# Kernel tuning notes

Measured on AMD Instinct MI355X. Metric: run time of the kernel, lower is better.

The kernel has to match this reference:

```python
import jax, jax.numpy as jnp
import numpy as np
import math

NUM_HEADS = 4
HIDDEN = 256
HEAD_DIM = HIDDEN // NUM_HEADS
NEG = jnp.finfo(jnp.float32).min


def setup_inputs() -> dict:
    key = jax.random.key(0)
    ks = jax.random.split(key, 8)
    B, Q, K = 4, 2048, 2048
    q_hidden_states = jax.random.normal(ks[0], (B, Q, HIDDEN), dtype=jnp.float32)
    k_hidden_states = jax.random.normal(ks[1], (B, K, HIDDEN), dtype=jnp.float32)
    attention_mask = jnp.zeros((B, 1, Q, K), dtype=jnp.float32)
    align_mask = jax.random.randint(ks[2], (B, K, Q), 0, 2, dtype=jnp.int32)
    s = 1.0 / math.sqrt(HIDDEN)
    Wq = jax.random.normal(ks[3], (HIDDEN, HIDDEN), dtype=jnp.float32) * s
    Wk = jax.random.normal(ks[4], (HIDDEN, HIDDEN), dtype=jnp.float32) * s
    Wv = jax.random.normal(ks[5], (HIDDEN, HIDDEN), dtype=jnp.float32) * s
    Wo = jax.random.normal(ks[6], (HIDDEN, HIDDEN), dtype=jnp.float32) * s
    return {"q_hidden_states": q_hidden_states, "k_hidden_states": k_hidden_states,
            "attention_mask": attention_mask, "align_mask": align_mask,
            "Wq": Wq, "Wk": Wk, "Wv": Wv, "Wo": Wo}


def reference(q_hidden_states, k_hidden_states, attention_mask, align_mask, Wq, Wk, Wv, Wo):
    B, Q, _ = q_hidden_states.shape
    K = k_hidden_states.shape[1]
    # torch Linear: y = x @ W.T  -> [B, S, H, D]
    q = (q_hidden_states @ Wq.T).reshape(B, Q, NUM_HEADS, HEAD_DIM)
    k = (k_hidden_states @ Wk.T).reshape(B, K, NUM_HEADS, HEAD_DIM)
    v = (k_hidden_states @ Wv.T).reshape(B, K, NUM_HEADS, HEAD_DIM)
    # scores: [B, H, Q, K]
    scores = jnp.einsum('bqhd,bkhd->bhqk', q, k) / math.sqrt(HEAD_DIM)
    # additive mask + clamp to finfo min
    scores = jnp.maximum(scores + attention_mask, NEG)
    # align_mask: (B, K, Q) -> (B, 1, Q, K); masked_fill where == 0
    am = jnp.transpose(align_mask, (0, 2, 1))[:, None, :, :]
    scores = jnp.where(am == 0, NEG, scores)
    scores = jnp.maximum(scores, NEG)
    probs = jax.nn.softmax(scores.astype(jnp.float32), axis=-1).astype(q.dtype)
    attn = jnp.einsum('bhqk,bkhd->bqhd', probs, v).reshape(B, Q, HIDDEN)
    return attn @ Wo.T
```

## Files before the change

kernel.cpp:

```cpp
#include <hip/hip_runtime.h>

#define NEGF -3.402823466e38f
#define MASKED_F -3.38953139e38f
#define LOG2E 1.44269504088896f
#define DEFER_THR 8.0f

typedef __attribute__((ext_vector_type(8))) short bf16x8;
typedef __attribute__((ext_vector_type(4))) float f32x4;
typedef __attribute__((ext_vector_type(4))) unsigned short u16x4;
typedef __attribute__((ext_vector_type(2))) unsigned int u32x2;

__device__ __forceinline__ unsigned short f2bf(float f) {
  unsigned u = __builtin_bit_cast(unsigned, f);
  u += 0x7fffu + ((u >> 16) & 1u);
  return (unsigned short)(u >> 16);
}

#define GLOAD_LDS16(gsrc, ldst)                                                     \
  __builtin_amdgcn_global_load_lds(                                                 \
      (const __attribute__((address_space(1))) void*)(gsrc),                        \
      (__attribute__((address_space(3))) void*)(ldst), 16, 0, 0)

#define OFF_QH  0u
#define OFF_KH  2097152u
#define OFF_W   4194304u
#define OFF_QP  4456448u
#define OFF_KP  6553600u
#define OFF_VT  8650752u
#define OFF_ATT 10747904u
#define OFF_BM  12845056u
#define OFF_FLAG 13893632u
#define USHORT_USED 13893664u

__global__ __launch_bounds__(256) void k_convert(
    const float* __restrict__ qh, const float* __restrict__ kh,
    const float* __restrict__ w0, const float* __restrict__ w1,
    const float* __restrict__ w2, const float* __restrict__ w3,
    unsigned short* __restrict__ dst) {
  int v = blockIdx.x * 256 + threadIdx.x;
  const float* src;
  if (v < 524288)       src = qh + (size_t)v * 4;
  else if (v < 1048576) src = kh + ((size_t)v - 524288) * 4;
  else {
    int t = v - 1048576;
    int which = t >> 14;
    const float* w = (which == 0) ? w0 : (which == 1) ? w1 : (which == 2) ? w2 : w3;
    src = w + (size_t)(t & 16383) * 4;
  }
  f32x4 x = *(const f32x4*)src;
  u16x4 o;
  o[0] = f2bf(x[0]); o[1] = f2bf(x[1]); o[2] = f2bf(x[2]); o[3] = f2bf(x[3]);
  *(u16x4*)(dst + (size_t)v * 4) = o;
}

__global__ __launch_bounds__(256) void k_bitpack(const int* __restrict__ al,
                                                 unsigned long long* __restrict__ bm,
                                                 int* __restrict__ flag) {
  int wi = blockIdx.x * 256 + threadIdx.x;
  if (wi == 0) *flag = 0;
  int q = wi & 2047;
  int k64 = (wi >> 11) & 31;
  int b = wi >> 16;
  const int* base = al + ((size_t)(b * 2048 + k64 * 64)) * 2048 + q;
  unsigned long long word = 0;
#pragma unroll
  for (int k = 0; k < 64; ++k)
    if (base[(size_t)k * 2048] != 0) word |= 1ull << k;
  bm[wi] = word;
}

__global__ __launch_bounds__(256) void k_amcheck(const float* __restrict__ am,
                                                 int* __restrict__ flag) {
  const f32x4* p = (const f32x4*)am;
  size_t tid = (size_t)blockIdx.x * 256 + threadIdx.x;
  unsigned nz = 0;
#pragma unroll
  for (int j = 0; j < 8; ++j) {
    f32x4 v = p[tid + (size_t)j * 524288];
    nz |= (v[0] != 0.f) | (v[1] != 0.f) | (v[2] != 0.f) | (v[3] != 0.f);
  }
  if (__any(nz)) {
    if ((threadIdx.x & 63) == 0) atomicOr(flag, 1);
  }
}

__global__ __launch_bounds__(256) void k_proj(unsigned short* __restrict__ ws) {
  int bid = blockIdx.x;
  int mat = bid / 512;
  int rem = bid - mat * 512;
  int mt = rem >> 2, nt = rem & 3;
  int tid = threadIdx.x, w = tid >> 6, lane = tid & 63;
  int l15 = lane & 15, l4 = lane >> 4;

  const unsigned short* X = ws + (mat == 0 ? OFF_QH : OFF_KH);
  const unsigned short* W = ws + OFF_W + (size_t)mat * 65536;

  int i0 = mt * 64 + w * 16;
  int arow = i0 + l15;
  int koff = l4 * 8;

  f32x4 acc[4] = {};
  for (int ks = 0; ks < 8; ++ks) {
    bf16x8 a = *(const bf16x8*)(X + (size_t)arow * 256 + ks * 32 + koff);
#pragma unroll
    for (int ct = 0; ct < 4; ++ct) {
      bf16x8 bb = *(const bf16x8*)(W + (size_t)(nt * 64 + ct * 16 + l15) * 256 + ks * 32 + koff);
      acc[ct] = __builtin_amdgcn_mfma_f32_16x16x32_bf16(a, bb, acc[ct], 0, 0, 0);
    }
  }

  unsigned short* Qp = ws + OFF_QP;
  unsigned short* Kp = ws + OFF_KP;
  unsigned short* Vt = ws + OFF_VT;
  int rbase = i0 + l4 * 4;
#pragma unroll
  for (int ct = 0; ct < 4; ++ct) {
#pragma unroll
    for (int r = 0; r < 4; ++r) {
      int row = rbase + r;
      int b = row >> 11, s = row & 2047;
      int d = ct * 16 + l15;
      float v = acc[ct][r];
      if (mat == 0)      Qp[((size_t)(b * 4 + nt) * 2048 + s) * 64 + d] = f2bf(v * (0.125f * LOG2E));
      else if (mat == 1) Kp[((size_t)(b * 4 + nt) * 2048 + s) * 64 + d] = f2bf(v);
      else               Vt[((size_t)(b * 4 + nt) * 64 + d) * 2048 + s] = f2bf(v);
    }
  }
}

template <int NS>
__global__ __launch_bounds__(256) void k_attn(unsigned short* __restrict__ ws,
    const float* __restrict__ am, const unsigned long long* __restrict__ bm,
    const int* __restrict__ amflag,
    float* __restrict__ po, float* __restrict__ pm, float* __restrict__ pl) {
  constexpr int LOG = (NS == 4) ? 2 : (NS == 2) ? 1 : 0;
  constexpr int SPAN = 2048 / NS;

  __shared__ __align__(16) unsigned short Kb[2][4096];
  __shared__ __align__(16) unsigned short Vb[2][4096];
  __shared__ __align__(16) unsigned short plds[4][1024];

  int bid = blockIdx.x;
  int sp = bid & (NS - 1);
  int qt = (bid >> LOG) & 31;
  int bh = bid >> (LOG + 5);
  int b = bh >> 2, h = bh & 3;
  int tid = threadIdx.x, w = tid >> 6, lane = tid & 63;
  int l15 = lane & 15, l4 = lane >> 4;
  int q0 = qt * 64 + w * 16;

  const bool hasam = (*amflag != 0);

  const unsigned short* Qp = ws + OFF_QP;
  const unsigned short* Kp = ws + OFF_KP + (size_t)bh * 2048 * 64;
  const unsigned short* Vt = ws + OFF_VT + (size_t)bh * 64 * 2048;
  const float* amq = am + ((size_t)(b * 2048 + q0 + l15)) * 2048;
  const unsigned long long* bmq = bm + (size_t)b * 65536 + q0 + l15;

  int srow = lane >> 3;
  int scol = ((lane & 7) ^ srow) * 8;
  int c0 = w * 2;

  bf16x8 qf0 = *(const bf16x8*)(Qp + ((size_t)bh * 2048 + q0 + l15) * 64 + l4 * 8);
  bf16x8 qf1 = *(const bf16x8*)(Qp + ((size_t)bh * 2048 + q0 + l15) * 64 + 32 + l4 * 8);

  f32x4 o[4] = {};
  float mrun = -__builtin_inff();
  float lpart = 0.f;
  int s0 = l4 * 4;

  int kk0 = sp * SPAN;
#pragma unroll
  for (int c2 = 0; c2 < 2; ++c2) {
    int c = c0 + c2;
    GLOAD_LDS16(Kp + (size_t)(kk0 + c * 8 + srow) * 64 + scol, &Kb[0][c * 512]);
    GLOAD_LDS16(Vt + (size_t)(c * 8 + srow) * 2048 + kk0 + scol, &Vb[0][c * 512]);
  }
  __syncthreads();

  int cur = 0;
  for (int kk = kk0; kk < kk0 + SPAN; kk += 64) {
    if (kk + 64 < kk0 + SPAN) {
#pragma unroll
      for (int c2 = 0; c2 < 2; ++c2) {
        int c = c0 + c2;
        GLOAD_LDS16(Kp + (size_t)(kk + 64 + c * 8 + srow) * 64 + scol, &Kb[cur ^ 1][c * 512]);
        GLOAD_LDS16(Vt + (size_t)(c * 8 + srow) * 2048 + (kk + 64) + scol, &Vb[cur ^ 1][c * 512]);
      }
    }
    unsigned long long wbits = bmq[(size_t)(kk >> 6) * 2048];
    unsigned blo = (unsigned)wbits, bhi = (unsigned)(wbits >> 32);
    f32x4 a0{}, a1{}, a2{}, a3{};
    if (hasam) {
      a0 = *(const f32x4*)(amq + kk + 0 * 16 + s0);
      a1 = *(const f32x4*)(amq + kk + 1 * 16 + s0);
      a2 = *(const f32x4*)(amq + kk + 2 * 16 + s0);
      a3 = *(const f32x4*)(amq + kk + 3 * 16 + s0);
    }

    f32x4 sfr[4];
    __builtin_amdgcn_s_setprio(1);
#pragma unroll
    for (int kt = 0; kt < 4; ++kt) {
      int row = kt * 16 + l15;
      int sw = l15 & 7;
      bf16x8 k0 = *(const bf16x8*)&Kb[cur][row * 64 + ((l4 ^ sw) * 8)];
      bf16x8 k1 = *(const bf16x8*)&Kb[cur][row * 64 + (((4 + l4) ^ sw) * 8)];
      f32x4 acc = {};
      acc = __builtin_amdgcn_mfma_f32_16x16x32_bf16(k0, qf0, acc, 0, 0, 0);
      acc = __builtin_amdgcn_mfma_f32_16x16x32_bf16(k1, qf1, acc, 0, 0, 0);
      sfr[kt] = acc;
    }
    __builtin_amdgcn_s_setprio(0);

#pragma unroll
    for (int kt = 0; kt < 4; ++kt) {
      unsigned half = (kt & 2) ? bhi : blo;
      int base = (kt & 1) ? 16 + s0 : s0;
      f32x4 a = (kt == 0) ? a0 : (kt == 1) ? a1 : (kt == 2) ? a2 : a3;
#pragma unroll
      for (int r = 0; r < 4; ++r) {
        float sc = sfr[kt][r];
        if (hasam) sc = fmaf(a[r], LOG2E, sc);
        sfr[kt][r] = ((half >> (base + r)) & 1u) ? sc : MASKED_F;
      }
    }

    float pmax = sfr[0][0];
#pragma unroll
    for (int kt = 0; kt < 4; ++kt)
#pragma unroll
      for (int r = 0; r < 4; ++r) pmax = fmaxf(pmax, sfr[kt][r]);
    pmax = fmaxf(pmax, __shfl_xor(pmax, 16));
    pmax = fmaxf(pmax, __shfl_xor(pmax, 32));

    if (__any(pmax > mrun + DEFER_THR)) {
      float mnew = fmaxf(mrun, pmax);
      float sfac = exp2f(mrun - mnew);
      mrun = mnew;
      lpart *= sfac;
#pragma unroll
      for (int r = 0; r < 4; ++r) {
        float sf = __shfl(sfac, l4 * 4 + r);
        o[0][r] *= sf; o[1][r] *= sf; o[2][r] *= sf; o[3][r] *= sf;
      }
    }

    float ls = 0.f;
#pragma unroll
    for (int kt = 0; kt < 4; ++kt)
#pragma unroll
      for (int r = 0; r < 4; ++r) {
        float e = exp2f(sfr[kt][r] - mrun);
        sfr[kt][r] = e;
        ls += e;
      }
    lpart += ls;

#pragma unroll
    for (int kt = 0; kt < 4; ++kt) {
      unsigned lo, hi;
      asm("v_cvt_pk_bf16_f32 %0, %1, %2" : "=v"(lo) : "v"(sfr[kt][0]), "v"(sfr[kt][1]));
      asm("v_cvt_pk_bf16_f32 %0, %1, %2" : "=v"(hi) : "v"(sfr[kt][2]), "v"(sfr[kt][3]));
      int chunk = kt * 2 + (l4 >> 1);
      int addr = l15 * 64 + (((chunk) ^ (l15 & 7)) << 3) + ((l4 & 1) << 2);
      u32x2 pk; pk[0] = lo; pk[1] = hi;
      *(u32x2*)&plds[w][addr] = pk;
    }

    __builtin_amdgcn_s_setprio(1);
#pragma unroll
    for (int ks = 0; ks < 2; ++ks) {
      int chnk = ks * 4 + l4;
      bf16x8 pa = *(const bf16x8*)&plds[w][l15 * 64 + ((chnk ^ (l15 & 7)) << 3)];
#pragma unroll
      for (int dt = 0; dt < 4; ++dt) {
        int row = dt * 16 + l15;
        bf16x8 vf = *(const bf16x8*)&Vb[cur][row * 64 + (((ks * 4 + l4) ^ (l15 & 7)) * 8)];
        o[dt] = __builtin_amdgcn_mfma_f32_16x16x32_bf16(pa, vf, o[dt], 0, 0, 0);
      }
    }
    __builtin_amdgcn_s_setprio(0);

    __syncthreads();
    cur ^= 1;
  }

  float lsum = lpart;
  lsum += __shfl_xor(lsum, 16);
  lsum += __shfl_xor(lsum, 32);

  if constexpr (NS == 1) {
    unsigned short* attnb = ws + OFF_ATT;
#pragma unroll
    for (int r = 0; r < 4; ++r) {
      float inv = 1.0f / __shfl(lsum, l4 * 4 + r);
      int qrow = q0 + l4 * 4 + r;
#pragma unroll
      for (int dt = 0; dt < 4; ++dt)
        attnb[(size_t)(b * 2048 + qrow) * 256 + h * 64 + dt * 16 + l15] = f2bf(o[dt][r] * inv);
    }
  } else {
    float* pob = po + (((size_t)sp * 16 + bh) * 2048) * 64;
#pragma unroll
    for (int r = 0; r < 4; ++r) {
      int qrow = q0 + l4 * 4 + r;
#pragma unroll
      for (int dt = 0; dt < 4; ++dt)
        pob[(size_t)qrow * 64 + dt * 16 + l15] = o[dt][r];
    }
    if (l4 == 0) {
      pm[(size_t)sp * 32768 + bh * 2048 + q0 + l15] = mrun;
      pl[(size_t)sp * 32768 + bh * 2048 + q0 + l15] = lsum;
    }
  }
}

template <int NS>
__global__ __launch_bounds__(256) void k_combine(const float* __restrict__ po,
    const float* __restrict__ pm, const float* __restrict__ pl,
    unsigned short* __restrict__ attnb) {
  int t = blockIdx.x * 256 + threadIdx.x;
  int d = t & 63;
  int row = t >> 6;

  float m[NS], l[NS];
  float M = -__builtin_inff();
#pragma unroll
  for (int sp = 0; sp < NS; ++sp) {
    m[sp] = pm[(size_t)sp * 32768 + row];
    l[sp] = pl[(size_t)sp * 32768 + row];
    M = fmaxf(M, m[sp]);
  }
  float denom = 0.f, acc = 0.f;
#pragma unroll
  for (int sp = 0; sp < NS; ++sp) {
    float wgt = exp2f(m[sp] - M);
    denom += l[sp] * wgt;
    acc += po[((size_t)sp * 32768 + row) * 64 + d] * wgt;
  }
  float val = acc / denom;
  int bh = row >> 11, qrow = row & 2047;
  int b = bh >> 2, h = bh & 3;
  attnb[((size_t)(b * 2048 + qrow)) * 256 + h * 64 + d] = f2bf(val);
}

__global__ __launch_bounds__(256) void k_oproj(const unsigned short* __restrict__ ws,
                                               float* __restrict__ out) {
  int bid = blockIdx.x;
  int mt = bid >> 2, nt = bid & 3;
  int tid = threadIdx.x, w = tid >> 6, lane = tid & 63;
  int l15 = lane & 15, l4 = lane >> 4;

  const unsigned short* A = ws + OFF_ATT;
  const unsigned short* W = ws + OFF_W + 3u * 65536u;
  int i0 = mt * 64 + w * 16;

  f32x4 acc[4] = {};
  for (int ks = 0; ks < 8; ++ks) {
    bf16x8 a = *(const bf16x8*)(A + (size_t)(i0 + l15) * 256 + ks * 32 + l4 * 8);
#pragma unroll
    for (int ct = 0; ct < 4; ++ct) {
      bf16x8 bb = *(const bf16x8*)(W + (size_t)(nt * 64 + ct * 16 + l15) * 256 + ks * 32 + l4 * 8);
      acc[ct] = __builtin_amdgcn_mfma_f32_16x16x32_bf16(a, bb, acc[ct], 0, 0, 0);
    }
  }
#pragma unroll
  for (int ct = 0; ct < 4; ++ct)
#pragma unroll
    for (int r = 0; r < 4; ++r)
      out[(size_t)(i0 + l4 * 4 + r) * 256 + nt * 64 + ct * 16 + l15] = acc[ct][r];
}

extern "C" void kernel_launch(void* const* d_in, const int* in_sizes, int n_in,
                              void* d_out, int out_size, void* d_ws, size_t ws_size,
                              hipStream_t stream) {
  const float* qh = (const float*)d_in[0];
  const float* kh = (const float*)d_in[1];
  const float* amask = (const float*)d_in[2];
  const int* alignm = (const int*)d_in[3];
  const float* Wq = (const float*)d_in[4];
  const float* Wk = (const float*)d_in[5];
  const float* Wv = (const float*)d_in[6];
  const float* Wo = (const float*)d_in[7];
  float* out = (float*)d_out;
  unsigned short* ws = (unsigned short*)d_ws;
  unsigned long long* bm = (unsigned long long*)(ws + OFF_BM);
  int* amflag = (int*)(ws + OFF_FLAG);

  k_convert<<<4352, 256, 0, stream>>>(qh, kh, Wq, Wk, Wv, Wo, ws);
  k_bitpack<<<1024, 256, 0, stream>>>(alignm, bm, amflag);
  k_amcheck<<<2048, 256, 0, stream>>>(amask, amflag);
  k_proj<<<1536, 256, 0, stream>>>(ws);

  size_t avail_f = (ws_size > (size_t)USHORT_USED * 2)
                       ? (ws_size - (size_t)USHORT_USED * 2) / 4 : 0;
  auto need = [](int ns) { return (size_t)ns * (2097152 + 65536); };
  int NSv = (avail_f >= need(2)) ? 2 : 1;
  float* po = (float*)(ws + USHORT_USED);
  float* pm = po + (size_t)NSv * 2097152;
  float* pl = pm + (size_t)NSv * 32768;

  if (NSv == 2) {
    k_attn<2><<<1024, 256, 0, stream>>>(ws, amask, bm, amflag, po, pm, pl);
    k_combine<2><<<8192, 256, 0, stream>>>(po, pm, pl, ws + OFF_ATT);
  } else {
    k_attn<1><<<512, 256, 0, stream>>>(ws, amask, bm, amflag, po, pm, pl);
  }
  k_oproj<<<512, 256, 0, stream>>>(ws, out);
}
```

Baseline: 140.3 us.

## Merge mask preprocessing kernels and apply align mask after exponentiation

Fuses the align-mask bitpack and attention-mask check into one kernel launch, with the flag reset moved into the convert kernel, which removes a launch and lets both workloads share the grid. In the attention loop the prefetch of the next K/V tile is moved after the mask and bias loads. The align mask is now applied by zeroing exp values with a bitmask after exp2, instead of selecting a large negative score before the max. This cuts per-element selects, but the running max now includes masked scores, which shifts the numerics and could underflow rows whose max comes from masked entries.

Result: faster. 129.5 us (-7.7%).

```diff
diff --git a/kernel.cpp b/kernel.cpp
--- a/kernel.cpp
+++ b/kernel.cpp
@@ -36,8 +36,9 @@
     const float* __restrict__ qh, const float* __restrict__ kh,
     const float* __restrict__ w0, const float* __restrict__ w1,
     const float* __restrict__ w2, const float* __restrict__ w3,
-    unsigned short* __restrict__ dst) {
+    unsigned short* __restrict__ dst, int* __restrict__ flag) {
   int v = blockIdx.x * 256 + threadIdx.x;
+  if (v == 0) *flag = 0;
   const float* src;
   if (v < 524288)       src = qh + (size_t)v * 4;
   else if (v < 1048576) src = kh + ((size_t)v - 524288) * 4;
@@ -53,34 +54,33 @@
   *(u16x4*)(dst + (size_t)v * 4) = o;
 }
 
-__global__ __launch_bounds__(256) void k_bitpack(const int* __restrict__ al,
-                                                 unsigned long long* __restrict__ bm,
-                                                 int* __restrict__ flag) {
-  int wi = blockIdx.x * 256 + threadIdx.x;
-  if (wi == 0) *flag = 0;
-  int q = wi & 2047;
-  int k64 = (wi >> 11) & 31;
-  int b = wi >> 16;
-  const int* base = al + ((size_t)(b * 2048 + k64 * 64)) * 2048 + q;
-  unsigned long long word = 0;
-#pragma unroll
-  for (int k = 0; k < 64; ++k)
-    if (base[(size_t)k * 2048] != 0) word |= 1ull << k;
-  bm[wi] = word;
-}
-
-__global__ __launch_bounds__(256) void k_amcheck(const float* __restrict__ am,
-                                                 int* __restrict__ flag) {
-  const f32x4* p = (const f32x4*)am;
-  size_t tid = (size_t)blockIdx.x * 256 + threadIdx.x;
-  unsigned nz = 0;
-#pragma unroll
-  for (int j = 0; j < 8; ++j) {
-    f32x4 v = p[tid + (size_t)j * 524288];
-    nz |= (v[0] != 0.f) | (v[1] != 0.f) | (v[2] != 0.f) | (v[3] != 0.f);
-  }
-  if (__any(nz)) {
-    if ((threadIdx.x & 63) == 0) atomicOr(flag, 1);
+__global__ __launch_bounds__(256) void k_maskaux(const int* __restrict__ al,
+    const float* __restrict__ am, unsigned long long* __restrict__ bm,
+    int* __restrict__ flag) {
+  int bid = blockIdx.x;
+  if (bid < 1024) {
+    int wi = bid * 256 + threadIdx.x;
+    int q = wi & 2047;
+    int k64 = (wi >> 11) & 31;
+    int b = wi >> 16;
+    const int* base = al + ((size_t)(b * 2048 + k64 * 64)) * 2048 + q;
+    unsigned long long word = 0;
+#pragma unroll
+    for (int k = 0; k < 64; ++k)
+      if (base[(size_t)k * 2048] != 0) word |= 1ull << k;
+    bm[wi] = word;
+  } else {
+    const f32x4* p = (const f32x4*)am;
+    size_t tid = (size_t)(bid - 1024) * 256 + threadIdx.x;
+    unsigned nz = 0;
+#pragma unroll
+    for (int j = 0; j < 16; ++j) {
+      f32x4 v = p[tid + (size_t)j * 262144];
+      nz |= (v[0] != 0.f) | (v[1] != 0.f) | (v[2] != 0.f) | (v[3] != 0.f);
+    }
+    if (__any(nz)) {
+      if ((threadIdx.x & 63) == 0) atomicOr(flag, 1);
+    }
   }
 }
 
@@ -180,22 +180,21 @@
 
   int cur = 0;
   for (int kk = kk0; kk < kk0 + SPAN; kk += 64) {
-    if (kk + 64 < kk0 + SPAN) {
-#pragma unroll
-      for (int c2 = 0; c2 < 2; ++c2) {
-        int c = c0 + c2;
-        GLOAD_LDS16(Kp + (size_t)(kk + 64 + c * 8 + srow) * 64 + scol, &Kb[cur ^ 1][c * 512]);
-        GLOAD_LDS16(Vt + (size_t)(c * 8 + srow) * 2048 + (kk + 64) + scol, &Vb[cur ^ 1][c * 512]);
-      }
-    }
     unsigned long long wbits = bmq[(size_t)(kk >> 6) * 2048];
-    unsigned blo = (unsigned)wbits, bhi = (unsigned)(wbits >> 32);
     f32x4 a0{}, a1{}, a2{}, a3{};
     if (hasam) {
       a0 = *(const f32x4*)(amq + kk + 0 * 16 + s0);
       a1 = *(const f32x4*)(amq + kk + 1 * 16 + s0);
       a2 = *(const f32x4*)(amq + kk + 2 * 16 + s0);
       a3 = *(const f32x4*)(amq + kk + 3 * 16 + s0);
+    }
+    if (kk + 64 < kk0 + SPAN) {
+#pragma unroll
+      for (int c2 = 0; c2 < 2; ++c2) {
+        int c = c0 + c2;
+        GLOAD_LDS16(Kp + (size_t)(kk + 64 + c * 8 + srow) * 64 + scol, &Kb[cur ^ 1][c * 512]);
+        GLOAD_LDS16(Vt + (size_t)(c * 8 + srow) * 2048 + (kk + 64) + scol, &Vb[cur ^ 1][c * 512]);
+      }
     }
 
     f32x4 sfr[4];
@@ -213,16 +212,12 @@
     }
     __builtin_amdgcn_s_setprio(0);
 
-#pragma unroll
-    for (int kt = 0; kt < 4; ++kt) {
-      unsigned half = (kt & 2) ? bhi : blo;
-      int base = (kt & 1) ? 16 + s0 : s0;
-      f32x4 a = (kt == 0) ? a0 : (kt == 1) ? a1 : (kt == 2) ? a2 : a3;
-#pragma unroll
-      for (int r = 0; r < 4; ++r) {
-        float sc = sfr[kt][r];
-        if (hasam) sc = fmaf(a[r], LOG2E, sc);
-        sfr[kt][r] = ((half >> (base + r)) & 1u) ? sc : MASKED_F;
+    if (hasam) {
+#pragma unroll
+      for (int kt = 0; kt < 4; ++kt) {
+        f32x4 a = (kt == 0) ? a0 : (kt == 1) ? a1 : (kt == 2) ? a2 : a3;
+#pragma unroll
+        for (int r = 0; r < 4; ++r) sfr[kt][r] = fmaf(a[r], LOG2E, sfr[kt][r]);
       }
     }
 
@@ -246,27 +241,28 @@
       }
     }
 
+    unsigned blo = (unsigned)wbits, bhi = (unsigned)(wbits >> 32);
     float ls = 0.f;
 #pragma unroll
-    for (int kt = 0; kt < 4; ++kt)
+    for (int kt = 0; kt < 4; ++kt) {
+      unsigned tbits = ((kt & 2) ? bhi : blo) >> ((kt & 1) ? 16 + s0 : s0);
+      float em[4];
 #pragma unroll
       for (int r = 0; r < 4; ++r) {
         float e = exp2f(sfr[kt][r] - mrun);
-        sfr[kt][r] = e;
-        ls += e;
+        unsigned keep = 0u - ((tbits >> r) & 1u);
+        em[r] = __builtin_bit_cast(float, __builtin_bit_cast(unsigned, e) & keep);
+        ls += em[r];
       }
-    lpart += ls;
-
-#pragma unroll
-    for (int kt = 0; kt < 4; ++kt) {
       unsigned lo, hi;
-      asm("v_cvt_pk_bf16_f32 %0, %1, %2" : "=v"(lo) : "v"(sfr[kt][0]), "v"(sfr[kt][1]));
-      asm("v_cvt_pk_bf16_f32 %0, %1, %2" : "=v"(hi) : "v"(sfr[kt][2]), "v"(sfr[kt][3]));
+      asm("v_cvt_pk_bf16_f32 %0, %1, %2" : "=v"(lo) : "v"(em[0]), "v"(em[1]));
+      asm("v_cvt_pk_bf16_f32 %0, %1, %2" : "=v"(hi) : "v"(em[2]), "v"(em[3]));
       int chunk = kt * 2 + (l4 >> 1);
       int addr = l15 * 64 + (((chunk) ^ (l15 & 7)) << 3) + ((l4 & 1) << 2);
       u32x2 pk; pk[0] = lo; pk[1] = hi;
       *(u32x2*)&plds[w][addr] = pk;
     }
+    lpart += ls;
 
     __builtin_amdgcn_s_setprio(1);
 #pragma unroll
@@ -388,9 +384,8 @@
   unsigned long long* bm = (unsigned long long*)(ws + OFF_BM);
   int* amflag = (int*)(ws + OFF_FLAG);
 
-  k_convert<<<4352, 256, 0, stream>>>(qh, kh, Wq, Wk, Wv, Wo, ws);
-  k_bitpack<<<1024, 256, 0, stream>>>(alignm, bm, amflag);
-  k_amcheck<<<2048, 256, 0, stream>>>(amask, amflag);
+  k_convert<<<4352, 256, 0, stream>>>(qh, kh, Wq, Wk, Wv, Wo, ws, amflag);
+  k_maskaux<<<2048, 256, 0, stream>>>(alignm, amask, bm, amflag);
   k_proj<<<1536, 256, 0, stream>>>(ws);
 
   size_t avail_f = (ws_size > (size_t)USHORT_USED * 2)
```
